# Kernel tuning notes

Measured on AMD Instinct MI355X. Metric: run time of the kernel, lower is better.

Reference implementation:

```python
import jax, jax.numpy as jnp
import numpy as np

V, D, H, L, E, DH, K, PMAX = 50257, 128, 4, 4, 8, 512, 2, 256
B, T = 8, 256


def setup_inputs() -> dict:
    key = jax.random.key(0)
    ks = jax.random.split(key, 10)
    s = 0.02
    def n(k, shape):
        return jax.random.normal(k, shape, jnp.float32) * s
    return dict(
        idx=jax.random.randint(ks[0], (B, T), 0, V),
        tok_emb=n(ks[1], (V, D)),
        pos_emb=n(ks[2], (PMAX, D)),
        ln1_g=jnp.ones((L, D), jnp.float32), ln1_b=jnp.zeros((L, D), jnp.float32),
        in_w=n(ks[3], (L, 3 * D, D)), in_b=jnp.zeros((L, 3 * D), jnp.float32),
        out_w=n(ks[4], (L, D, D)), out_b=jnp.zeros((L, D), jnp.float32),
        ln2_g=jnp.ones((L, D), jnp.float32), ln2_b=jnp.zeros((L, D), jnp.float32),
        gate_w=n(ks[5], (L, E, D)),
        w1=n(ks[6], (L, E, DH, D)),
        w2=n(ks[7], (L, E, D, DH)),
        lnf_g=jnp.ones((D,), jnp.float32), lnf_b=jnp.zeros((D,), jnp.float32),
        lm_w=n(ks[8], (V, D)),
    )


def _ln(x, g, b):
    mu = x.mean(-1, keepdims=True)
    var = jnp.var(x, -1, keepdims=True)
    return (x - mu) / jnp.sqrt(var + 1e-5) * g + b


def _moe(x, gw, w1, w2):
    # x: [N, D]; top-2 sparse MoE, computed densely per expert then combined.
    logits = x @ gw.T                              # [N, E]
    probs = jax.nn.softmax(logits, -1)
    topw, topi = jax.lax.top_k(probs, K)           # [N, K]
    topw = topw / topw.sum(-1, keepdims=True)
    we = (topw[..., None] * jax.nn.one_hot(topi, E, dtype=x.dtype)).sum(1)  # [N, E]
    h = jax.nn.silu(jnp.einsum('nd,ehd->neh', x, w1))   # [N, E, DH]
    y = jnp.einsum('neh,edh->ned', h, w2)               # [N, E, D]
    return jnp.einsum('ned,ne->nd', y, we)


def reference(idx, tok_emb, pos_emb, ln1_g, ln1_b, in_w, in_b, out_w, out_b,
              ln2_g, ln2_b, gate_w, w1, w2, lnf_g, lnf_b, lm_w):
    b, t = idx.shape
    x = tok_emb[idx] + pos_emb[:t]                 # [B, T, D]
    dh = D // H
    scale = 1.0 / np.sqrt(dh)
    for l in range(L):
        xl = _ln(x, ln1_g[l], ln1_b[l])
        qkv = xl @ in_w[l].T + in_b[l]
        q, k, v = jnp.split(qkv, 3, -1)
        q = q.reshape(b, t, H, dh)
        k = k.reshape(b, t, H, dh)
        v = v.reshape(b, t, H, dh)
        att = jax.nn.softmax(jnp.einsum('bqhd,bkhd->bhqk', q, k) * scale, -1)
        o = jnp.einsum('bhqk,bkhd->bqhd', att, v).reshape(b, t, D)
        x = x + o @ out_w[l].T + out_b[l]
        x2 = _ln(x, ln2_g[l], ln2_b[l]).reshape(b * t, D)
        x = x + _moe(x2, gate_w[l], w1[l], w2[l]).reshape(b, t, D)
    return _ln(x, lnf_g, lnf_b) @ lm_w.T           # [B, T, V]
```

## Files before the change

kernel.cpp:

```cpp
#include <hip/hip_runtime.h>
#include <math.h>

#define NTOK 2048
#define DD   128
#define NHEAD 4
#define DHEAD 32
#define NLAYER 4
#define NEXP 8
#define DHID 512
#define NVOCAB 50257
#define VPAD  50304
#define SEQ   256
#define NBATCH 8

typedef __attribute__((ext_vector_type(8))) short short8v;
typedef __attribute__((ext_vector_type(4))) float f32x4;

__device__ __forceinline__ unsigned short nm_bf16r(float f) {
  unsigned u = __float_as_uint(f);
  u += 0x7fffu + ((u >> 16) & 1u);
  return (unsigned short)(u >> 16);
}

__device__ __forceinline__ float nm_silu(float a) {
  return a / (1.f + __expf(-a));
}

template<int N4>
__device__ __forceinline__ float nm_dotv(const float* __restrict__ a,
                                         const float* __restrict__ w) {
  const float4* a4 = (const float4*)a;
  const float4* w4 = (const float4*)w;
  float sx = 0.f, sy = 0.f, sz = 0.f, sw = 0.f;
#pragma unroll 16
  for (int k = 0; k < N4; ++k) {
    float4 av = a4[k], wv = w4[k];
    sx = fmaf(av.x, wv.x, sx);
    sy = fmaf(av.y, wv.y, sy);
    sz = fmaf(av.z, wv.z, sz);
    sw = fmaf(av.w, wv.w, sw);
  }
  return (sx + sy) + (sz + sw);
}

#define C3_LMW 6438912ull
#define C3_W1  6963200ull
#define C3_ALL 7487488ull
#define CVTB   7312
__global__ __launch_bounds__(256) void nm_init(
    const int* __restrict__ idx, const float* __restrict__ tok,
    const float* __restrict__ pos, const float* __restrict__ g,
    const float* __restrict__ b, const float* __restrict__ lmw,
    const float* __restrict__ w1l3, const float* __restrict__ w2l3,
    float* __restrict__ x, float* __restrict__ xl,
    unsigned short* __restrict__ lmwb, unsigned short* __restrict__ w1b3,
    unsigned short* __restrict__ w2b3, int* __restrict__ zp) {
  int bid = blockIdx.x, tid = threadIdx.x;
  if (bid < CVTB) {
    size_t base = ((size_t)bid * 256 + tid) * 4;
    if (base < (size_t)NVOCAB * DD) {
      float4 v = *(const float4*)(lmw + base);
      ushort4 us = {nm_bf16r(v.x), nm_bf16r(v.y), nm_bf16r(v.z), nm_bf16r(v.w)};
      *(ushort4*)(lmwb + base) = us;
    } else if (base < C3_LMW) {
      ushort4 us = {0, 0, 0, 0};
      *(ushort4*)(lmwb + base) = us;
    } else if (base < C3_W1) {
      size_t j = base - C3_LMW;
      float4 v = *(const float4*)(w1l3 + j);
      ushort4 us = {nm_bf16r(v.x), nm_bf16r(v.y), nm_bf16r(v.z), nm_bf16r(v.w)};
      *(ushort4*)(w1b3 + j) = us;
    } else {
      size_t j = base - C3_W1;
      float4 v = *(const float4*)(w2l3 + j);
      ushort4 us = {nm_bf16r(v.x), nm_bf16r(v.y), nm_bf16r(v.z), nm_bf16r(v.w)};
      *(ushort4*)(w2b3 + j) = us;
    }
  } else if (bid < CVTB + NTOK / 4) {
    int n = (bid - CVTB) * 4 + (tid >> 6);
    int lane = tid & 63;
    int t = idx[n];
    float v0 = tok[(size_t)t * DD + lane]      + pos[(n % SEQ) * DD + lane];
    float v1 = tok[(size_t)t * DD + lane + 64] + pos[(n % SEQ) * DD + lane + 64];
    x[n * DD + lane]      = v0;
    x[n * DD + lane + 64] = v1;
    float s = v0 + v1;
#pragma unroll
    for (int o = 32; o > 0; o >>= 1) s += __shfl_xor(s, o, 64);
    float mu = s * (1.f / 128.f);
    float d0 = v0 - mu, d1 = v1 - mu;
    float q = d0 * d0 + d1 * d1;
#pragma unroll
    for (int o = 32; o > 0; o >>= 1) q += __shfl_xor(q, o, 64);
    float rstd = rsqrtf(q * (1.f / 128.f) + 1e-5f);
    xl[n * DD + lane]      = d0 * rstd * g[lane]      + b[lane];
    xl[n * DD + lane + 64] = d1 * rstd * g[lane + 64] + b[lane + 64];
  } else {
    if (tid < 72) zp[tid] = 0;
  }
}

__global__ void nm_embed_ln(const int* __restrict__ idx, const float* __restrict__ tok,
                            const float* __restrict__ pos, const float* __restrict__ g,
                            const float* __restrict__ b, float* __restrict__ x,
                            float* __restrict__ xlf) {
  int n = blockIdx.x, lane = threadIdx.x;
  int t = idx[n];
  float v0 = tok[(size_t)t * DD + lane]      + pos[(n % SEQ) * DD + lane];
  float v1 = tok[(size_t)t * DD + lane + 64] + pos[(n % SEQ) * DD + lane + 64];
  x[n * DD + lane]      = v0;
  x[n * DD + lane + 64] = v1;
  float s = v0 + v1;
#pragma unroll
  for (int o = 32; o > 0; o >>= 1) s += __shfl_xor(s, o, 64);
  float mu = s * (1.f / 128.f);
  float d0 = v0 - mu, d1 = v1 - mu;
  float q = d0 * d0 + d1 * d1;
#pragma unroll
  for (int o = 32; o > 0; o >>= 1) q += __shfl_xor(q, o, 64);
  float rstd = rsqrtf(q * (1.f / 128.f) + 1e-5f);
  xlf[n * DD + lane]      = d0 * rstd * g[lane]      + b[lane];
  xlf[n * DD + lane + 64] = d1 * rstd * g[lane + 64] + b[lane + 64];
}

__global__ void nm_ln(const float* __restrict__ in, const float* __restrict__ g,
                      const float* __restrict__ b, float* __restrict__ out) {
  int n = blockIdx.x, lane = threadIdx.x;
  float v0 = in[n * DD + lane], v1 = in[n * DD + lane + 64];
  float s = v0 + v1;
#pragma unroll
  for (int o = 32; o > 0; o >>= 1) s += __shfl_xor(s, o, 64);
  float mu = s * (1.f / 128.f);
  float d0 = v0 - mu, d1 = v1 - mu;
  float q = d0 * d0 + d1 * d1;
#pragma unroll
  for (int o = 32; o > 0; o >>= 1) q += __shfl_xor(q, o, 64);
  float rstd = rsqrtf(q * (1.f / 128.f) + 1e-5f);
  out[n * DD + lane]      = d0 * rstd * g[lane]      + b[lane];
  out[n * DD + lane + 64] = d1 * rstd * g[lane + 64] + b[lane + 64];
}

__global__ void nm_combine_ln(const float* __restrict__ yb, const int* __restrict__ posm,
                              const float* __restrict__ topw, float* __restrict__ x,
                              const float* __restrict__ g, const float* __restrict__ b,
                              float* __restrict__ xl, unsigned short* __restrict__ xb) {
  int n = blockIdx.x, lane = threadIdx.x;
  float w0 = topw[2 * n], w1 = topw[2 * n + 1];
  int p0 = posm[2 * n], p1 = posm[2 * n + 1];
  float v0 = x[n * DD + lane]      + w0 * yb[(size_t)p0 * DD + lane]
                                   + w1 * yb[(size_t)p1 * DD + lane];
  float v1 = x[n * DD + lane + 64] + w0 * yb[(size_t)p0 * DD + lane + 64]
                                   + w1 * yb[(size_t)p1 * DD + lane + 64];
  x[n * DD + lane]      = v0;
  x[n * DD + lane + 64] = v1;
  float s = v0 + v1;
#pragma unroll
  for (int o = 32; o > 0; o >>= 1) s += __shfl_xor(s, o, 64);
  float mu = s * (1.f / 128.f);
  float d0 = v0 - mu, d1 = v1 - mu;
  float q = d0 * d0 + d1 * d1;
#pragma unroll
  for (int o = 32; o > 0; o >>= 1) q += __shfl_xor(q, o, 64);
  float rstd = rsqrtf(q * (1.f / 128.f) + 1e-5f);
  float o0 = d0 * rstd * g[lane]      + b[lane];
  float o1 = d1 * rstd * g[lane + 64] + b[lane + 64];
  xl[n * DD + lane]      = o0;
  xl[n * DD + lane + 64] = o1;
  if (xb) {
    xb[n * DD + lane]      = nm_bf16r(o0);
    xb[n * DD + lane + 64] = nm_bf16r(o1);
  }
}

template<int F, int MT>
__global__ __launch_bounds__(256) void nm_gemm2(
    const float* __restrict__ A, const float* __restrict__ B,
    float* __restrict__ C, const float* __restrict__ bias,
    int M, int N, int K,
    const int* __restrict__ list, const int* __restrict__ cnt,
    const int* __restrict__ off) {
  constexpr bool GA = F & 1, SI = F & 2, BI = F & 4, GR = F & 16;
  constexpr int RG = MT / 64;
  __shared__ __align__(16) float As[64][MT + 4];
  __shared__ __align__(16) float Bs[64][68];
  int tid = threadIdx.x;
  int n0 = blockIdx.x * 64, m0 = blockIdx.y * MT;
  int Mloc = M, o = 0;
  const float* Bb = B;
  if constexpr (GR) {
    int e = blockIdx.z;
    Mloc = cnt[e];
    if (m0 >= Mloc) return;
    o = off[e];
    Bb = B + (size_t)e * (size_t)N * K;
  }
  int tm = tid & 15, tn = tid >> 4;
  float acc[RG * 4][4] = {};
  for (int kc = 0; kc < K; kc += 64) {
#pragma unroll
    for (int i = 0; i < RG * 4; ++i) {
      int f = tid + 256 * i;
      int r = f >> 4, c4 = f & 15;
      int mi = m0 + r;
      if (mi >= Mloc) mi = m0;
      const float* ar;
      if constexpr (GA) ar = A + (size_t)(list[o + mi] >> 1) * K;
      else              ar = A + (size_t)(o + mi) * K;
      float4 v = *(const float4*)(ar + kc + c4 * 4);
      int k = c4 * 4;
      As[k][r] = v.x; As[k + 1][r] = v.y; As[k + 2][r] = v.z; As[k + 3][r] = v.w;
    }
#pragma unroll
    for (int i = 0; i < 4; ++i) {
      int f = tid + 256 * i;
      int r = f >> 4, c4 = f & 15;
      const float* br = Bb + (size_t)(n0 + r) * K + kc + c4 * 4;
      float4 v = *(const float4*)br;
      int k = c4 * 4;
      Bs[k][r] = v.x; Bs[k + 1][r] = v.y; Bs[k + 2][r] = v.z; Bs[k + 3][r] = v.w;
    }
    __syncthreads();
#pragma unroll 16
    for (int k = 0; k < 64; ++k) {
      float4 b = *(const float4*)&Bs[k][tn * 4];
#pragma unroll
      for (int g2 = 0; g2 < RG; ++g2) {
        float4 a = *(const float4*)&As[k][g2 * 64 + tm * 4];
        acc[g2*4+0][0] = fmaf(a.x, b.x, acc[g2*4+0][0]);
        acc[g2*4+0][1] = fmaf(a.x, b.y, acc[g2*4+0][1]);
        acc[g2*4+0][2] = fmaf(a.x, b.z, acc[g2*4+0][2]);
        acc[g2*4+0][3] = fmaf(a.x, b.w, acc[g2*4+0][3]);
        acc[g2*4+1][0] = fmaf(a.y, b.x, acc[g2*4+1][0]);
        acc[g2*4+1][1] = fmaf(a.y, b.y, acc[g2*4+1][1]);
        acc[g2*4+1][2] = fmaf(a.y, b.z, acc[g2*4+1][2]);
        acc[g2*4+1][3] = fmaf(a.y, b.w, acc[g2*4+1][3]);
        acc[g2*4+2][0] = fmaf(a.z, b.x, acc[g2*4+2][0]);
        acc[g2*4+2][1] = fmaf(a.z, b.y, acc[g2*4+2][1]);
        acc[g2*4+2][2] = fmaf(a.z, b.z, acc[g2*4+2][2]);
        acc[g2*4+2][3] = fmaf(a.z, b.w, acc[g2*4+2][3]);
        acc[g2*4+3][0] = fmaf(a.w, b.x, acc[g2*4+3][0]);
        acc[g2*4+3][1] = fmaf(a.w, b.y, acc[g2*4+3][1]);
        acc[g2*4+3][2] = fmaf(a.w, b.z, acc[g2*4+3][2]);
        acc[g2*4+3][3] = fmaf(a.w, b.w, acc[g2*4+3][3]);
      }
    }
    __syncthreads();
  }
  float4 bv = {0.f, 0.f, 0.f, 0.f};
  if constexpr (BI) bv = *(const float4*)(bias + n0 + tn * 4);
#pragma unroll
  for (int g2 = 0; g2 < RG; ++g2) {
#pragma unroll
    for (int i = 0; i < 4; ++i) {
      int row = m0 + g2 * 64 + tm * 4 + i;
      if (GR && row >= Mloc) continue;
      float* cr = C + (size_t)(o + row) * N + n0 + tn * 4;
      float r0 = acc[g2 * 4 + i][0], r1 = acc[g2 * 4 + i][1];
      float r2 = acc[g2 * 4 + i][2], r3 = acc[g2 * 4 + i][3];
      if constexpr (BI) { r0 += bv.x; r1 += bv.y; r2 += bv.z; r3 += bv.w; }
      if constexpr (SI) { r0 = nm_silu(r0); r1 = nm_silu(r1); r2 = nm_silu(r2); r3 = nm_silu(r3); }
      float4 st = {r0, r1, r2, r3};
      *(float4*)cr = st;
    }
  }
}

template<int F, int KK>
__global__ __launch_bounds__(256) void nm_bgemm(
    const unsigned short* __restrict__ A, const unsigned short* __restrict__ B,
    float* __restrict__ Cf, unsigned short* __restrict__ Cb,
    const float* __restrict__ bias, int M, int N,
    const int* __restrict__ list, const int* __restrict__ cnt,
    const int* __restrict__ off) {
  constexpr bool GA = F & 1, SI = F & 2, BI = F & 4, SB = F & 8, GR = F & 16;
  int wave = threadIdx.x >> 6, lane = threadIdx.x & 63;
  int n0 = blockIdx.x * 32;
  int m0 = blockIdx.y * 128 + wave * 32;
  int Mloc = M, o = 0;
  const unsigned short* Bb = B;
  if constexpr (GR) {
    int e = blockIdx.z;
    Mloc = cnt[e];
    o = off[e];
    Bb = B + (size_t)e * (size_t)N * KK;
  }
  if (m0 >= Mloc) return;
  int lr = lane & 15, lk = (lane >> 4) * 8;
  const unsigned short* arow[2];
#pragma unroll
  for (int i = 0; i < 2; ++i) {
    int mi = m0 + i * 16 + lr;
    if (mi >= Mloc) mi = Mloc - 1;
    int r = GA ? (list[o + mi] >> 1) : (o + mi);
    arow[i] = A + (size_t)r * KK;
  }
  const unsigned short* brow[2] = { Bb + (size_t)(n0 + lr) * KK,
                                    Bb + (size_t)(n0 + 16 + lr) * KK };
  f32x4 acc[2][2] = {};
#pragma unroll
  for (int ks = 0; ks < KK / 32; ++ks) {
    int kb = ks * 32 + lk;
    short8v a0 = *(const short8v*)(arow[0] + kb);
    short8v a1 = *(const short8v*)(arow[1] + kb);
    short8v b0 = *(const short8v*)(brow[0] + kb);
    short8v b1 = *(const short8v*)(brow[1] + kb);
    acc[0][0] = __builtin_amdgcn_mfma_f32_16x16x32_bf16(a0, b0, acc[0][0], 0, 0, 0);
    acc[0][1] = __builtin_amdgcn_mfma_f32_16x16x32_bf16(a0, b1, acc[0][1], 0, 0, 0);
    acc[1][0] = __builtin_amdgcn_mfma_f32_16x16x32_bf16(a1, b0, acc[1][0], 0, 0, 0);
    acc[1][1] = __builtin_amdgcn_mfma_f32_16x16x32_bf16(a1, b1, acc[1][1], 0, 0, 0);
  }
  float bc[2] = {0.f, 0.f};
  if constexpr (BI) {
    bc[0] = bias[n0 + (lane & 15)];
    bc[1] = bias[n0 + 16 + (lane & 15)];
  }
#pragma unroll
  for (int i = 0; i < 2; ++i) {
    int rbase = m0 + i * 16 + (lane >> 4) * 4;
#pragma unroll
    for (int r = 0; r < 4; ++r) {
      int row = rbase + r;
      if (GR && row >= Mloc) continue;
#pragma unroll
      for (int j = 0; j < 2; ++j) {
        float v = acc[i][j][r];
        if constexpr (BI) v += bc[j];
        if constexpr (SI) v = nm_silu(v);
        int col = n0 + j * 16 + (lane & 15);
        if constexpr (SB) Cb[(size_t)(o + row) * N + col] = nm_bf16r(v);
        else              Cf[(size_t)(o + row) * N + col] = v;
      }
    }
  }
}

__global__ __launch_bounds__(256) void nm_oplng(
    const float* __restrict__ ao, const float* __restrict__ w,
    const float* __restrict__ bias, float* __restrict__ x,
    const float* __restrict__ g, const float* __restrict__ b,
    float* __restrict__ xl, unsigned short* __restrict__ xlb,
    const float* __restrict__ gw,
    int* __restrict__ topi, float* __restrict__ topw, int* __restrict__ cnt,
    int* __restrict__ ticket, int* __restrict__ off, int* __restrict__ list,
    int* __restrict__ posm) {
  __shared__ __align__(16) float As[64][36];
  __shared__ __align__(16) float Bs[64][132];
  __shared__ float Ls[32][9];
  __shared__ int doR;
  __shared__ int cv[NEXP], lcur[NEXP];
  int tid = threadIdx.x;
  int m0 = blockIdx.x * 32;
  int tm = tid >> 5, tn = tid & 31;
  float acc[4][4] = {};
  for (int kc = 0; kc < DD; kc += 64) {
#pragma unroll
    for (int i = 0; i < 2; ++i) {
      int ch = tid + 256 * i, r = ch >> 4, c4 = ch & 15;
      float4 v = *(const float4*)(ao + (size_t)(m0 + r) * DD + kc + c4 * 4);
      int k = c4 * 4;
      As[k][r] = v.x; As[k + 1][r] = v.y; As[k + 2][r] = v.z; As[k + 3][r] = v.w;
    }
#pragma unroll
    for (int i = 0; i < 8; ++i) {
      int ch = tid + 256 * i, r = ch >> 4, c4 = ch & 15;
      float4 v = *(const float4*)(w + (size_t)r * DD + kc + c4 * 4);
      int k = c4 * 4;
      Bs[k][r] = v.x; Bs[k + 1][r] = v.y; Bs[k + 2][r] = v.z; Bs[k + 3][r] = v.w;
    }
    __syncthreads();
#pragma unroll 8
    for (int k = 0; k < 64; ++k) {
      float4 a = *(const float4*)&As[k][tm * 4];
      float4 bb = *(const float4*)&Bs[k][tn * 4];
      acc[0][0] = fmaf(a.x, bb.x, acc[0][0]); acc[0][1] = fmaf(a.x, bb.y, acc[0][1]);
      acc[0][2] = fmaf(a.x, bb.z, acc[0][2]); acc[0][3] = fmaf(a.x, bb.w, acc[0][3]);
      acc[1][0] = fmaf(a.y, bb.x, acc[1][0]); acc[1][1] = fmaf(a.y, bb.y, acc[1][1]);
      acc[1][2] = fmaf(a.y, bb.z, acc[1][2]); acc[1][3] = fmaf(a.y, bb.w, acc[1][3]);
      acc[2][0] = fmaf(a.z, bb.x, acc[2][0]); acc[2][1] = fmaf(a.z, bb.y, acc[2][1]);
      acc[2][2] = fmaf(a.z, bb.z, acc[2][2]); acc[2][3] = fmaf(a.z, bb.w, acc[2][3]);
      acc[3][0] = fmaf(a.w, bb.x, acc[3][0]); acc[3][1] = fmaf(a.w, bb.y, acc[3][1]);
      acc[3][2] = fmaf(a.w, bb.z, acc[3][2]); acc[3][3] = fmaf(a.w, bb.w, acc[3][3]);
    }
    __syncthreads();
  }
  float4 bv = *(const float4*)(bias + tn * 4);
  float rr[4][4], s1[4], s2[4];
#pragma unroll
  for (int i = 0; i < 4; ++i) {
    int rw = m0 + tm * 4 + i;
    float4 xv = *(const float4*)(x + (size_t)rw * DD + tn * 4);
    float r0 = acc[i][0] + bv.x + xv.x;
    float r1 = acc[i][1] + bv.y + xv.y;
    float r2 = acc[i][2] + bv.z + xv.z;
    float r3 = acc[i][3] + bv.w + xv.w;
    rr[i][0] = r0; rr[i][1] = r1; rr[i][2] = r2; rr[i][3] = r3;
    float4 st = {r0, r1, r2, r3};
    *(float4*)(x + (size_t)rw * DD + tn * 4) = st;
    s1[i] = r0 + r1 + r2 + r3;
    s2[i] = r0 * r0 + r1 * r1 + r2 * r2 + r3 * r3;
  }
#pragma unroll
  for (int o = 16; o >= 1; o >>= 1) {
#pragma unroll
    for (int i = 0; i < 4; ++i) {
      s1[i] += __shfl_xor(s1[i], o, 64);
      s2[i] += __shfl_xor(s2[i], o, 64);
    }
  }
  float4 gv  = *(const float4*)(g + tn * 4);
  float4 bbv = *(const float4*)(b + tn * 4);
#pragma unroll
  for (int i = 0; i < 4; ++i) {
    int rw = m0 + tm * 4 + i;
    float mu = s1[i] * (1.f / 128.f);
    float var = s2[i] * (1.f / 128.f) - mu * mu;
    float rstd = rsqrtf(var + 1e-5f);
    float y0 = (rr[i][0] - mu) * rstd * gv.x + bbv.x;
    float y1 = (rr[i][1] - mu) * rstd * gv.y + bbv.y;
    float y2 = (rr[i][2] - mu) * rstd * gv.z + bbv.z;
    float y3 = (rr[i][3] - mu) * rstd * gv.w + bbv.w;
    float4 yv = {y0, y1, y2, y3};
    *(float4*)(xl + (size_t)rw * DD + tn * 4) = yv;
    if (xlb) {
      ushort4 us = {nm_bf16r(y0), nm_bf16r(y1), nm_bf16r(y2), nm_bf16r(y3)};
      *(ushort4*)(xlb + (size_t)rw * DD + tn * 4) = us;
    }
    *(float4*)&Bs[tm * 4 + i][tn * 4] = yv;
  }
  __syncthreads();
  int grow = tid >> 3, ge = tid & 7;
  const float4* xr = (const float4*)&Bs[grow][0];
  const float4* wr = (const float4*)(gw + (size_t)ge * DD);
  float sx = 0.f, sy = 0.f, sz = 0.f, sw = 0.f;
#pragma unroll
  for (int k2 = 0; k2 < 32; ++k2) {
    float4 a = xr[k2], w4 = wr[k2];
    sx = fmaf(a.x, w4.x, sx); sy = fmaf(a.y, w4.y, sy);
    sz = fmaf(a.z, w4.z, sz); sw = fmaf(a.w, w4.w, sw);
  }
  Ls[grow][ge] = (sx + sy) + (sz + sw);
  __syncthreads();
  if (ge == 0) {
    float gl[NEXP];
#pragma unroll
    for (int e = 0; e < NEXP; ++e) gl[e] = Ls[grow][e];
    int i0 = 0;
#pragma unroll
    for (int e = 1; e < NEXP; ++e) if (gl[e] > gl[i0]) i0 = e;
    int i1 = (i0 == 0) ? 1 : 0;
#pragma unroll
    for (int e = 0; e < NEXP; ++e) { if (e != i0 && gl[e] > gl[i1]) i1 = e; }
    float p1 = __expf(gl[i1] - gl[i0]);
    float inv = 1.f / (1.f + p1);
    int n = m0 + grow;
    topi[2 * n] = i0; topi[2 * n + 1] = i1;
    topw[2 * n] = inv; topw[2 * n + 1] = p1 * inv;
    atomicAdd(cnt + i0, 1);
    atomicAdd(cnt + i1, 1);
  }
  __syncthreads();
  if (tid == 0) {
    __threadfence();
    doR = (atomicAdd(ticket, 1) == 63);
    if (doR) __threadfence();
  }
  __syncthreads();
  if (doR) {
    if (tid < NEXP) cv[tid] = atomicAdd(cnt + tid, 0);
    __syncthreads();
    if (tid < NEXP) {
      int o2 = 0;
      for (int e = 0; e < tid; ++e) o2 += cv[e];
      lcur[tid] = o2;
      off[tid] = o2;
    }
    __syncthreads();
    for (int t = tid; t < 2 * NTOK; t += 256) {
      int e = topi[t];
      int p = atomicAdd(&lcur[e], 1);
      list[p] = t;
      posm[t] = p;
    }
  }
}

__global__ __launch_bounds__(256) void nm_attn3(const float* __restrict__ qkv,
                                                float* __restrict__ o) {
  __shared__ __align__(16) float smem[2 * SEQ * DHEAD];
  float4* K4 = (float4*)smem;
  float4* V4 = (float4*)(smem + SEQ * DHEAD);
  int bh = blockIdx.x;
  int b = bh >> 2, h = bh & 3;
  int qt = blockIdx.y;
  int tid = threadIdx.x;
  const float* base = qkv + (size_t)b * SEQ * 384;
  for (int f = tid; f < SEQ * 8; f += 256) {
    int t = f >> 3, c4 = f & 7;
    int pc = (c4 + (t >> 4)) & 7;
    K4[t * 8 + pc] = *(const float4*)(base + (size_t)t * 384 + 128 + h * DHEAD + c4 * 4);
    V4[t * 8 + pc] = *(const float4*)(base + (size_t)t * 384 + 256 + h * DHEAD + c4 * 4);
  }
  __syncthreads();
  int qi = tid >> 4, slot = tid & 15;
  int tq = qt * 16 + qi;
  float qv[DHEAD];
  const float4* q4 = (const float4*)(base + (size_t)tq * 384 + h * DHEAD);
#pragma unroll
  for (int k = 0; k < 8; ++k) {
    float4 v = q4[k];
    qv[4*k] = v.x; qv[4*k+1] = v.y; qv[4*k+2] = v.z; qv[4*k+3] = v.w;
  }
  float m = -1e30f, s = 0.f, acc[DHEAD];
#pragma unroll
  for (int d = 0; d < DHEAD; ++d) acc[d] = 0.f;
  const float scale = 0.17677669529663687f;
  int sw = slot & 7;
  for (int jj = 0; jj < 16; ++jj) {
    int j = slot * 16 + jj;
    float sc = 0.f;
#pragma unroll
    for (int k = 0; k < 8; ++k) {
      float4 v = K4[j * 8 + ((k + sw) & 7)];
      sc += qv[4*k]*v.x + qv[4*k+1]*v.y + qv[4*k+2]*v.z + qv[4*k+3]*v.w;
    }
    sc *= scale;
    float mn = fmaxf(m, sc);
    float f = __expf(m - mn), p = __expf(sc - mn);
    s = s * f + p;
#pragma unroll
    for (int k = 0; k < 8; ++k) {
      float4 v = V4[j * 8 + ((k + sw) & 7)];
      acc[4*k]   = acc[4*k]  * f + p * v.x;
      acc[4*k+1] = acc[4*k+1]* f + p * v.y;
      acc[4*k+2] = acc[4*k+2]* f + p * v.z;
      acc[4*k+3] = acc[4*k+3]* f + p * v.w;
    }
    m = mn;
  }
  __syncthreads();
  float* cb = smem;
  float* my = cb + (qi * 16 + slot) * 34;
#pragma unroll
  for (int d = 0; d < DHEAD; ++d) my[d] = acc[d];
  my[32] = m;
  my[33] = s;
  __syncthreads();
  int q2 = tid >> 4, dg = tid & 15;
  const float* qb = cb + q2 * 16 * 34;
  float M = qb[32];
#pragma unroll
  for (int t = 1; t < 16; ++t) M = fmaxf(M, qb[t * 34 + 32]);
  float S = 0.f, v0 = 0.f, v1 = 0.f;
#pragma unroll
  for (int t = 0; t < 16; ++t) {
    float w = __expf(qb[t * 34 + 32] - M);
    S += qb[t * 34 + 33] * w;
    v0 += w * qb[t * 34 + dg * 2];
    v1 += w * qb[t * 34 + dg * 2 + 1];
  }
  float inv = 1.f / S;
  float* orow = o + (size_t)(b * SEQ + qt * 16 + q2) * DD + h * DHEAD + dg * 2;
  orow[0] = v0 * inv;
  orow[1] = v1 * inv;
}

__global__ void nm_qkv(const float* __restrict__ xl, const float* __restrict__ w,
                       const float* __restrict__ bias, float* __restrict__ qkv) {
  __shared__ __align__(16) float xs[DD];
  int n = blockIdx.x, tid = threadIdx.x;
  xs[tid] = xl[n * DD + tid];
  __syncthreads();
#pragma unroll
  for (int jj = 0; jj < 3; ++jj) {
    int j = tid + jj * 128;
    qkv[(size_t)n * 384 + j] = nm_dotv<32>(xs, w + (size_t)j * DD) + bias[j];
  }
}

__global__ void nm_outproj(const float* __restrict__ ao, const float* __restrict__ w,
                           const float* __restrict__ bias, float* __restrict__ x) {
  __shared__ __align__(16) float os[DD];
  int n = blockIdx.x, tid = threadIdx.x;
  os[tid] = ao[n * DD + tid];
  __syncthreads();
  x[n * DD + tid] += nm_dotv<32>(os, w + (size_t)tid * DD) + bias[tid];
}

__global__ void nm_moe(const float* __restrict__ x2, const float* __restrict__ gw,
                       const float* __restrict__ w1, const float* __restrict__ w2,
                       float* __restrict__ x) {
  __shared__ __align__(16) float xs[DD];
  __shared__ __align__(16) float hs[DHID];
  __shared__ float gl[NEXP];
  __shared__ int   ei[2];
  __shared__ float ew[2];
  int n = blockIdx.x, tid = threadIdx.x;
  if (tid < DD) xs[tid] = x2[n * DD + tid];
  __syncthreads();
  if (tid < NEXP) gl[tid] = nm_dotv<32>(xs, gw + (size_t)tid * DD);
  __syncthreads();
  if (tid == 0) {
    int i0 = 0;
#pragma unroll
    for (int e = 1; e < NEXP; ++e) if (gl[e] > gl[i0]) i0 = e;
    int i1 = (i0 == 0) ? 1 : 0;
    for (int e = 0; e < NEXP; ++e) { if (e == i0) continue; if (gl[e] > gl[i1]) i1 = e; }
    float p1 = __expf(gl[i1] - gl[i0]);
    float inv = 1.f / (1.f + p1);
    ei[0] = i0; ei[1] = i1; ew[0] = inv; ew[1] = p1 * inv;
  }
  __syncthreads();
  float yacc = 0.f;
  for (int t2 = 0; t2 < 2; ++t2) {
    int e = ei[t2];
    float wt = ew[t2];
    const float* w1e = w1 + (size_t)e * DHID * DD;
#pragma unroll
    for (int jj = 0; jj < 2; ++jj) {
      int j = tid + jj * 256;
      float a = nm_dotv<32>(xs, w1e + (size_t)j * DD);
      hs[j] = nm_silu(a);
    }
    __syncthreads();
    if (tid < DD) yacc += wt * nm_dotv<128>(hs, w2 + ((size_t)e * DD + tid) * DHID);
    __syncthreads();
  }
  if (tid < DD) x[n * DD + tid] += yacc;
}

__device__ __forceinline__ short8v nm_cvt8(const float* p) {
  const float4* p4 = (const float4*)p;
  float4 a = p4[0], b = p4[1];
  short8v r;
  r[0] = (short)nm_bf16r(a.x); r[1] = (short)nm_bf16r(a.y);
  r[2] = (short)nm_bf16r(a.z); r[3] = (short)nm_bf16r(a.w);
  r[4] = (short)nm_bf16r(b.x); r[5] = (short)nm_bf16r(b.y);
  r[6] = (short)nm_bf16r(b.z); r[7] = (short)nm_bf16r(b.w);
  return r;
}

__global__ __launch_bounds__(256) void nm_lmhead_f32(
    const float* __restrict__ xf, const float* __restrict__ lmw,
    float* __restrict__ out) {
  int wave = threadIdx.x >> 6, lane = threadIdx.x & 63;
  int wr = wave >> 1, wc = wave & 1;
  int row0 = blockIdx.y * 128 + wr * 64;
  int col0 = blockIdx.x * 128 + wc * 64;
  int lr = lane & 15, lk = (lane >> 4) * 8;
  f32x4 acc[4][4] = {};
#pragma unroll
  for (int ks = 0; ks < 4; ++ks) {
    int kb = ks * 32 + lk;
    short8v a[4], b[4];
#pragma unroll
    for (int i = 0; i < 4; ++i)
      a[i] = nm_cvt8(xf + (size_t)(row0 + i * 16 + lr) * DD + kb);
#pragma unroll
    for (int j = 0; j < 4; ++j) {
      int c = col0 + j * 16 + lr;
      if (c < NVOCAB) b[j] = nm_cvt8(lmw + (size_t)c * DD + kb);
      else {
        short8v z;
#pragma unroll
        for (int e = 0; e < 8; ++e) z[e] = 0;
        b[j] = z;
      }
    }
#pragma unroll
    for (int i = 0; i < 4; ++i)
#pragma unroll
      for (int j = 0; j < 4; ++j)
        acc[i][j] = __builtin_amdgcn_mfma_f32_16x16x32_bf16(a[i], b[j], acc[i][j], 0, 0, 0);
  }
  int cr = (lane >> 4) * 4;
#pragma unroll
  for (int j = 0; j < 4; ++j) {
    int c = col0 + j * 16 + (lane & 15);
    if (c < NVOCAB) {
#pragma unroll
      for (int i = 0; i < 4; ++i)
#pragma unroll
        for (int r = 0; r < 4; ++r)
          out[(size_t)(row0 + i * 16 + cr + r) * NVOCAB + c] = acc[i][j][r];
    }
  }
}

__global__ __launch_bounds__(256) void nm_lmhead2(
    const unsigned short* __restrict__ xfb, const unsigned short* __restrict__ lmwb,
    float* __restrict__ out) {
  __shared__ __align__(16) unsigned char smem[132 * 128 * 4];
  unsigned short* Ab = (unsigned short*)smem;
  unsigned short* Bb = Ab + 128 * 128;
  int tid = threadIdx.x;
  int row0 = blockIdx.y * 128, col0 = blockIdx.x * 128;
#pragma unroll
  for (int i = 0; i < 8; ++i) {
    int ch = tid + i * 256;
    int r = ch >> 4, s = ch & 15;
    int sg = s ^ (r & 7);
    *(short8v*)&Ab[r * 128 + s * 8] =
        *(const short8v*)(xfb + (size_t)(row0 + r) * DD + sg * 8);
    *(short8v*)&Bb[r * 128 + s * 8] =
        *(const short8v*)(lmwb + (size_t)(col0 + r) * DD + sg * 8);
  }
  __syncthreads();
  int wave = tid >> 6, lane = tid & 63;
  int wr = wave >> 1, wc = wave & 1;
  int lr = lane & 15, hk = lane >> 4;
  f32x4 acc[4][4] = {};
#pragma unroll
  for (int ks = 0; ks < 4; ++ks) {
    int sg = ks * 4 + hk;
    int sx = (sg ^ (lr & 7)) * 8;
    short8v a[4], b[4];
#pragma unroll
    for (int i = 0; i < 4; ++i)
      a[i] = *(const short8v*)&Ab[(wr * 64 + i * 16 + lr) * 128 + sx];
#pragma unroll
    for (int j = 0; j < 4; ++j)
      b[j] = *(const short8v*)&Bb[(wc * 64 + j * 16 + lr) * 128 + sx];
#pragma unroll
    for (int i = 0; i < 4; ++i)
#pragma unroll
      for (int j = 0; j < 4; ++j)
        acc[i][j] = __builtin_amdgcn_mfma_f32_16x16x32_bf16(a[i], b[j], acc[i][j], 0, 0, 0);
  }
  __syncthreads();
  float* Cs = (float*)smem;
  int hi4 = hk * 4;
#pragma unroll
  for (int j = 0; j < 4; ++j)
#pragma unroll
    for (int i = 0; i < 4; ++i)
#pragma unroll
      for (int r = 0; r < 4; ++r)
        Cs[(wr * 64 + i * 16 + hi4 + r) * 132 + wc * 64 + j * 16 + lr] = acc[i][j][r];
  __syncthreads();
  bool full = (col0 + 128 <= NVOCAB);
#pragma unroll 4
  for (int rr = 0; rr < 32; ++rr) {
    int row = wave * 32 + rr;
    float v0 = Cs[row * 132 + lane];
    float v1 = Cs[row * 132 + 64 + lane];
    size_t base = (size_t)(row0 + row) * NVOCAB + col0;
    if (full) {
      out[base + lane] = v0;
      out[base + 64 + lane] = v1;
    } else {
      if (col0 + lane < NVOCAB)      out[base + lane] = v0;
      if (col0 + 64 + lane < NVOCAB) out[base + 64 + lane] = v1;
    }
  }
}

extern "C" void kernel_launch(void* const* d_in, const int* in_sizes, int n_in,
                              void* d_out, int out_size, void* d_ws, size_t ws_size,
                              hipStream_t stream) {
  const int*   idx   = (const int*)  d_in[0];
  const float* tok   = (const float*)d_in[1];
  const float* pos   = (const float*)d_in[2];
  const float* ln1g  = (const float*)d_in[3];
  const float* ln1b  = (const float*)d_in[4];
  const float* inw   = (const float*)d_in[5];
  const float* inb   = (const float*)d_in[6];
  const float* outw  = (const float*)d_in[7];
  const float* outb  = (const float*)d_in[8];
  const float* ln2g  = (const float*)d_in[9];
  const float* ln2b  = (const float*)d_in[10];
  const float* gatew = (const float*)d_in[11];
  const float* w1    = (const float*)d_in[12];
  const float* w2    = (const float*)d_in[13];
  const float* lnfg  = (const float*)d_in[14];
  const float* lnfb  = (const float*)d_in[15];
  const float* lmw   = (const float*)d_in[16];
  float* out = (float*)d_out;

  float* ws   = (float*)d_ws;
  float* x    = ws;
  float* xl   = x    + NTOK * DD;
  float* qkv  = xl   + NTOK * DD;
  float* ao   = qkv  + NTOK * 384;
  float* topw = ao   + NTOK * DD;
  float* H    = topw + 2 * NTOK;
  float* yb   = H    + 2 * NTOK * DHID;
  int*   topi = (int*)(yb + 2 * NTOK * DD);
  int*   list = topi + 2 * NTOK;
  int*   posm = list + 2 * NTOK;
  int*   cnt  = posm + 2 * NTOK;
  int*   offs = cnt  + NLAYER * NEXP;
  int*   tick = offs + NLAYER * NEXP;
  unsigned short* xlb  = (unsigned short*)(tick + 8);
  unsigned short* Hb   = xlb + NTOK * DD;
  unsigned short* xfb  = Hb  + 2 * NTOK * DHID;
  unsigned short* w1b3 = xfb + NTOK * DD;
  unsigned short* w2b3 = w1b3 + NEXP * DHID * DD;
  unsigned short* lmwb = w2b3 + NEXP * DD * DHID;
  const size_t need = (size_t)((char*)(lmwb + (size_t)VPAD * DD) - (char*)d_ws);
  const bool pre = (ws_size >= need);

  const float* w1l3 = w1 + (size_t)3 * NEXP * DHID * DD;
  const float* w2l3 = w2 + (size_t)3 * NEXP * DD * DHID;

  if (pre) {
    nm_init<<<CVTB + NTOK / 4 + 1, 256, 0, stream>>>(
        idx, tok, pos, ln1g, ln1b, lmw, w1l3, w2l3, x, xl, lmwb, w1b3, w2b3, cnt);
    for (int l = 0; l < NLAYER; ++l) {
      nm_gemm2<4, 64><<<dim3(384 / 64, NTOK / 64), 256, 0, stream>>>(
          xl, inw + (size_t)l * 384 * DD, qkv, inb + (size_t)l * 384,
          NTOK, 384, DD, nullptr, nullptr, nullptr);
      nm_attn3<<<dim3(NBATCH * NHEAD, SEQ / 16), 256, 0, stream>>>(qkv, ao);
      nm_oplng<<<NTOK / 32, 256, 0, stream>>>(
          ao, outw + (size_t)l * DD * DD, outb + (size_t)l * DD, x,
          ln2g + l * DD, ln2b + l * DD, xl, (l == 3) ? xlb : (unsigned short*)nullptr,
          gatew + (size_t)l * NEXP * DD, topi, topw, cnt + l * NEXP,
          tick + l, offs + l * NEXP, list, posm);
      int* cnt_l = cnt + l * NEXP;
      int* off_l = offs + l * NEXP;
      if (l < 3) {
        const float* w1l = w1 + (size_t)l * NEXP * DHID * DD;
        const float* w2l = w2 + (size_t)l * NEXP * DD * DHID;
        nm_gemm2<19, 64><<<dim3(DHID / 64, 2 * NTOK / 64, NEXP), 256, 0, stream>>>(
            xl, w1l, H, nullptr, 0, DHID, DD, list, cnt_l, off_l);
        nm_gemm2<16, 64><<<dim3(DD / 64, 2 * NTOK / 64, NEXP), 256, 0, stream>>>(
            H, w2l, yb, nullptr, 0, DD, DHID, nullptr, cnt_l, off_l);
      } else {
        nm_bgemm<27, 128><<<dim3(DHID / 32, 32, NEXP), 256, 0, stream>>>(
            xlb, w1b3, nullptr, Hb, nullptr, 0, DHID, list, cnt_l, off_l);
        nm_bgemm<16, 512><<<dim3(DD / 32, 32, NEXP), 256, 0, stream>>>(
            Hb, w2b3, yb, nullptr, nullptr, 0, DD, nullptr, cnt_l, off_l);
      }
      const float* gN = (l < NLAYER - 1) ? ln1g + (l + 1) * DD : lnfg;
      const float* bN = (l < NLAYER - 1) ? ln1b + (l + 1) * DD : lnfb;
      nm_combine_ln<<<NTOK, 64, 0, stream>>>(
          yb, posm, topw, x, gN, bN, xl,
          (l == NLAYER - 1) ? xfb : (unsigned short*)nullptr);
    }
    nm_lmhead2<<<dim3(VPAD / 128, NTOK / 128), 256, 0, stream>>>(xfb, lmwb, out);
  } else {
    nm_embed_ln<<<NTOK, 64, 0, stream>>>(idx, tok, pos, ln1g, ln1b, x, xl);
    for (int l = 0; l < NLAYER; ++l) {
      nm_qkv<<<NTOK, 128, 0, stream>>>(xl, inw + (size_t)l * 384 * DD,
                                       inb + (size_t)l * 384, qkv);
      nm_attn3<<<dim3(NBATCH * NHEAD, SEQ / 16), 256, 0, stream>>>(qkv, ao);
      nm_outproj<<<NTOK, 128, 0, stream>>>(ao, outw + (size_t)l * DD * DD,
                                           outb + (size_t)l * DD, x);
      nm_ln<<<NTOK, 64, 0, stream>>>(x, ln2g + l * DD, ln2b + l * DD, xl);
      nm_moe<<<NTOK, 256, 0, stream>>>(xl, gatew + (size_t)l * NEXP * DD,
                                       w1 + (size_t)l * NEXP * DHID * DD,
                                       w2 + (size_t)l * NEXP * DD * DHID, x);
      const float* gN = (l < NLAYER - 1) ? ln1g + (l + 1) * DD : lnfg;
      const float* bN = (l < NLAYER - 1) ? ln1b + (l + 1) * DD : lnfb;
      nm_ln<<<NTOK, 64, 0, stream>>>(x, gN, bN, xl);
    }
    nm_lmhead_f32<<<dim3(VPAD / 128, NTOK / 128), 256, 0, stream>>>(xl, lmw, out);
  }
}
```

Baseline: 766.9 us.

## Fuse MoE combine and next-layer LayerNorm into the QKV projection kernel

Replaces the separate combine+LN kernel and the following QKV GEMM with one templated kernel. It applies the top-2 expert combine, computes LayerNorm over 32-token tiles in registers, and computes the 384-wide QKV projection from shared memory. Mode 0 handles the first layer from the precomputed LN output, and mode 2 handles the final LN with bf16 output. This removes one launch per layer and the global round trip of the normalized activations. In exchange the projection uses a scalar fp32 dot product per output instead of the tiled GEMM, and LayerNorm now uses a one-pass variance formula.

```diff
diff --git a/kernel.cpp b/kernel.cpp
--- a/kernel.cpp
+++ b/kernel.cpp
@@ -100,75 +100,100 @@
   }
 }
 
-__global__ void nm_embed_ln(const int* __restrict__ idx, const float* __restrict__ tok,
-                            const float* __restrict__ pos, const float* __restrict__ g,
-                            const float* __restrict__ b, float* __restrict__ x,
-                            float* __restrict__ xlf) {
-  int n = blockIdx.x, lane = threadIdx.x;
-  int t = idx[n];
-  float v0 = tok[(size_t)t * DD + lane]      + pos[(n % SEQ) * DD + lane];
-  float v1 = tok[(size_t)t * DD + lane + 64] + pos[(n % SEQ) * DD + lane + 64];
-  x[n * DD + lane]      = v0;
-  x[n * DD + lane + 64] = v1;
-  float s = v0 + v1;
-#pragma unroll
-  for (int o = 32; o > 0; o >>= 1) s += __shfl_xor(s, o, 64);
-  float mu = s * (1.f / 128.f);
-  float d0 = v0 - mu, d1 = v1 - mu;
-  float q = d0 * d0 + d1 * d1;
-#pragma unroll
-  for (int o = 32; o > 0; o >>= 1) q += __shfl_xor(q, o, 64);
-  float rstd = rsqrtf(q * (1.f / 128.f) + 1e-5f);
-  xlf[n * DD + lane]      = d0 * rstd * g[lane]      + b[lane];
-  xlf[n * DD + lane + 64] = d1 * rstd * g[lane + 64] + b[lane + 64];
-}
-
-__global__ void nm_ln(const float* __restrict__ in, const float* __restrict__ g,
-                      const float* __restrict__ b, float* __restrict__ out) {
-  int n = blockIdx.x, lane = threadIdx.x;
-  float v0 = in[n * DD + lane], v1 = in[n * DD + lane + 64];
-  float s = v0 + v1;
-#pragma unroll
-  for (int o = 32; o > 0; o >>= 1) s += __shfl_xor(s, o, 64);
-  float mu = s * (1.f / 128.f);
-  float d0 = v0 - mu, d1 = v1 - mu;
-  float q = d0 * d0 + d1 * d1;
-#pragma unroll
-  for (int o = 32; o > 0; o >>= 1) q += __shfl_xor(q, o, 64);
-  float rstd = rsqrtf(q * (1.f / 128.f) + 1e-5f);
-  out[n * DD + lane]      = d0 * rstd * g[lane]      + b[lane];
-  out[n * DD + lane + 64] = d1 * rstd * g[lane + 64] + b[lane + 64];
-}
-
-__global__ void nm_combine_ln(const float* __restrict__ yb, const int* __restrict__ posm,
-                              const float* __restrict__ topw, float* __restrict__ x,
-                              const float* __restrict__ g, const float* __restrict__ b,
-                              float* __restrict__ xl, unsigned short* __restrict__ xb) {
-  int n = blockIdx.x, lane = threadIdx.x;
-  float w0 = topw[2 * n], w1 = topw[2 * n + 1];
-  int p0 = posm[2 * n], p1 = posm[2 * n + 1];
-  float v0 = x[n * DD + lane]      + w0 * yb[(size_t)p0 * DD + lane]
-                                   + w1 * yb[(size_t)p1 * DD + lane];
-  float v1 = x[n * DD + lane + 64] + w0 * yb[(size_t)p0 * DD + lane + 64]
-                                   + w1 * yb[(size_t)p1 * DD + lane + 64];
-  x[n * DD + lane]      = v0;
-  x[n * DD + lane + 64] = v1;
-  float s = v0 + v1;
-#pragma unroll
-  for (int o = 32; o > 0; o >>= 1) s += __shfl_xor(s, o, 64);
-  float mu = s * (1.f / 128.f);
-  float d0 = v0 - mu, d1 = v1 - mu;
-  float q = d0 * d0 + d1 * d1;
-#pragma unroll
-  for (int o = 32; o > 0; o >>= 1) q += __shfl_xor(q, o, 64);
-  float rstd = rsqrtf(q * (1.f / 128.f) + 1e-5f);
-  float o0 = d0 * rstd * g[lane]      + b[lane];
-  float o1 = d1 * rstd * g[lane + 64] + b[lane + 64];
-  xl[n * DD + lane]      = o0;
-  xl[n * DD + lane + 64] = o1;
-  if (xb) {
-    xb[n * DD + lane]      = nm_bf16r(o0);
-    xb[n * DD + lane + 64] = nm_bf16r(o1);
+template<int MODE>
+__global__ __launch_bounds__(256) void nm_cqkv(
+    const float* __restrict__ yb, const int* __restrict__ posm,
+    const float* __restrict__ topw, float* __restrict__ x,
+    const float* __restrict__ xlin, const float* __restrict__ g,
+    const float* __restrict__ b, unsigned short* __restrict__ xfb,
+    const float* __restrict__ w, const float* __restrict__ bias,
+    float* __restrict__ qkv) {
+  __shared__ __align__(16) float xs[32][132];
+  __shared__ __align__(16) float qs[(MODE < 2) ? 32 * 388 : 4];
+  int tid = threadIdx.x;
+  int n0 = blockIdx.x * 32;
+  int r = tid >> 3, p = tid & 7;
+  int n = n0 + r;
+  float4 a0, a1, a2, a3;
+  if constexpr (MODE == 0) {
+    const float* xr = xlin + (size_t)n * DD + p * 16;
+    a0 = *(const float4*)(xr + 0);  a1 = *(const float4*)(xr + 4);
+    a2 = *(const float4*)(xr + 8);  a3 = *(const float4*)(xr + 12);
+#pragma unroll
+    for (int i = 0; i < 4; ++i) {
+      ((float4*)&xs[r][p * 16])[i] = (i == 0) ? a0 : (i == 1) ? a1 : (i == 2) ? a2 : a3;
+    }
+  } else {
+    float* xr = x + (size_t)n * DD + p * 16;
+    a0 = *(const float4*)(xr + 0);  a1 = *(const float4*)(xr + 4);
+    a2 = *(const float4*)(xr + 8);  a3 = *(const float4*)(xr + 12);
+    float w0 = topw[2 * n], w1 = topw[2 * n + 1];
+    int p0 = posm[2 * n], p1 = posm[2 * n + 1];
+    const float* y0 = yb + (size_t)p0 * DD + p * 16;
+    const float* y1 = yb + (size_t)p1 * DD + p * 16;
+#pragma unroll
+    for (int i = 0; i < 4; ++i) {
+      float4 u0 = ((const float4*)y0)[i];
+      float4 u1 = ((const float4*)y1)[i];
+      float4* ai = (i == 0) ? &a0 : (i == 1) ? &a1 : (i == 2) ? &a2 : &a3;
+      ai->x += w0 * u0.x + w1 * u1.x;
+      ai->y += w0 * u0.y + w1 * u1.y;
+      ai->z += w0 * u0.z + w1 * u1.z;
+      ai->w += w0 * u0.w + w1 * u1.w;
+    }
+    if constexpr (MODE == 1) {
+      ((float4*)xr)[0] = a0; ((float4*)xr)[1] = a1;
+      ((float4*)xr)[2] = a2; ((float4*)xr)[3] = a3;
+    }
+    float s1 = (a0.x + a0.y + a0.z + a0.w) + (a1.x + a1.y + a1.z + a1.w)
+             + (a2.x + a2.y + a2.z + a2.w) + (a3.x + a3.y + a3.z + a3.w);
+    float s2 = a0.x*a0.x + a0.y*a0.y + a0.z*a0.z + a0.w*a0.w
+             + a1.x*a1.x + a1.y*a1.y + a1.z*a1.z + a1.w*a1.w
+             + a2.x*a2.x + a2.y*a2.y + a2.z*a2.z + a2.w*a2.w
+             + a3.x*a3.x + a3.y*a3.y + a3.z*a3.z + a3.w*a3.w;
+#pragma unroll
+    for (int o = 4; o >= 1; o >>= 1) {
+      s1 += __shfl_xor(s1, o, 8);
+      s2 += __shfl_xor(s2, o, 8);
+    }
+    float mu = s1 * (1.f / 128.f);
+    float var = s2 * (1.f / 128.f) - mu * mu;
+    float rstd = rsqrtf(var + 1e-5f);
+    const float4* gp = (const float4*)(g + p * 16);
+    const float4* bp = (const float4*)(b + p * 16);
+#pragma unroll
+    for (int i = 0; i < 4; ++i) {
+      float4 gv = gp[i], bv = bp[i];
+      float4* ai = (i == 0) ? &a0 : (i == 1) ? &a1 : (i == 2) ? &a2 : &a3;
+      float4 yv = {(ai->x - mu) * rstd * gv.x + bv.x,
+                   (ai->y - mu) * rstd * gv.y + bv.y,
+                   (ai->z - mu) * rstd * gv.z + bv.z,
+                   (ai->w - mu) * rstd * gv.w + bv.w};
+      if constexpr (MODE == 2) {
+        ushort4 us = {nm_bf16r(yv.x), nm_bf16r(yv.y), nm_bf16r(yv.z), nm_bf16r(yv.w)};
+        *(ushort4*)(xfb + (size_t)n * DD + p * 16 + i * 4) = us;
+      } else {
+        ((float4*)&xs[r][p * 16])[i] = yv;
+      }
+    }
+  }
+  if constexpr (MODE == 2) return;
+  __syncthreads();
+  float* qsf = (float*)qs;
+#pragma unroll 8
+  for (int i = 0; i < 48; ++i) {
+    int pp = i * 256 + tid;
+    int col = pp >> 5, tk = pp & 31;
+    float v = nm_dotv<32>(&xs[tk][0], w + (size_t)col * DD) + bias[col];
+    qsf[tk * 388 + col] = v;
+  }
+  __syncthreads();
+#pragma unroll
+  for (int i = 0; i < 12; ++i) {
+    int e4 = i * 256 + tid;
+    int tk = e4 / 96, c4 = e4 % 96;
+    float4 v = *(const float4*)&qsf[tk * 388 + c4 * 4];
+    *(float4*)(qkv + (size_t)(n0 + tk) * 384 + c4 * 4) = v;
   }
 }
 
@@ -562,6 +587,46 @@
   float* orow = o + (size_t)(b * SEQ + qt * 16 + q2) * DD + h * DHEAD + dg * 2;
   orow[0] = v0 * inv;
   orow[1] = v1 * inv;
+}
+
+__global__ void nm_embed_ln(const int* __restrict__ idx, const float* __restrict__ tok,
+                            const float* __restrict__ pos, const float* __restrict__ g,
+                            const float* __restrict__ b, float* __restrict__ x,
+                            float* __restrict__ xlf) {
+  int n = blockIdx.x, lane = threadIdx.x;
+  int t = idx[n];
+  float v0 = tok[(size_t)t * DD + lane]      + pos[(n % SEQ) * DD + lane];
+  float v1 = tok[(size_t)t * DD + lane + 64] + pos[(n % SEQ) * DD + lane + 64];
+  x[n * DD + lane]      = v0;
+  x[n * DD + lane + 64] = v1;
+  float s = v0 + v1;
+#pragma unroll
+  for (int o = 32; o > 0; o >>= 1) s += __shfl_xor(s, o, 64);
+  float mu = s * (1.f / 128.f);
+  float d0 = v0 - mu, d1 = v1 - mu;
+  float q = d0 * d0 + d1 * d1;
+#pragma unroll
+  for (int o = 32; o > 0; o >>= 1) q += __shfl_xor(q, o, 64);
+  float rstd = rsqrtf(q * (1.f / 128.f) + 1e-5f);
+  xlf[n * DD + lane]      = d0 * rstd * g[lane]      + b[lane];
+  xlf[n * DD + lane + 64] = d1 * rstd * g[lane + 64] + b[lane + 64];
+}
+
+__global__ void nm_ln(const float* __restrict__ in, const float* __restrict__ g,
+                      const float* __restrict__ b, float* __restrict__ out) {
+  int n = blockIdx.x, lane = threadIdx.x;
+  float v0 = in[n * DD + lane], v1 = in[n * DD + lane + 64];
+  float s = v0 + v1;
+#pragma unroll
+  for (int o = 32; o > 0; o >>= 1) s += __shfl_xor(s, o, 64);
+  float mu = s * (1.f / 128.f);
+  float d0 = v0 - mu, d1 = v1 - mu;
+  float q = d0 * d0 + d1 * d1;
+#pragma unroll
+  for (int o = 32; o > 0; o >>= 1) q += __shfl_xor(q, o, 64);
+  float rstd = rsqrtf(q * (1.f / 128.f) + 1e-5f);
+  out[n * DD + lane]      = d0 * rstd * g[lane]      + b[lane];
+  out[n * DD + lane + 64] = d1 * rstd * g[lane + 64] + b[lane + 64];
 }
 
 __global__ void nm_qkv(const float* __restrict__ xl, const float* __restrict__ w,
@@ -805,10 +870,10 @@
   if (pre) {
     nm_init<<<CVTB + NTOK / 4 + 1, 256, 0, stream>>>(
         idx, tok, pos, ln1g, ln1b, lmw, w1l3, w2l3, x, xl, lmwb, w1b3, w2b3, cnt);
+    nm_cqkv<0><<<NTOK / 32, 256, 0, stream>>>(
+        nullptr, nullptr, nullptr, x, xl, nullptr, nullptr, nullptr,
+        inw, inb, qkv);
     for (int l = 0; l < NLAYER; ++l) {
-      nm_gemm2<4, 64><<<dim3(384 / 64, NTOK / 64), 256, 0, stream>>>(
-          xl, inw + (size_t)l * 384 * DD, qkv, inb + (size_t)l * 384,
-          NTOK, 384, DD, nullptr, nullptr, nullptr);
       nm_attn3<<<dim3(NBATCH * NHEAD, SEQ / 16), 256, 0, stream>>>(qkv, ao);
       nm_oplng<<<NTOK / 32, 256, 0, stream>>>(
           ao, outw + (size_t)l * DD * DD, outb + (size_t)l * DD, x,
@@ -830,11 +895,15 @@
         nm_bgemm<16, 512><<<dim3(DD / 32, 32, NEXP), 256, 0, stream>>>(
             Hb, w2b3, yb, nullptr, nullptr, 0, DD, nullptr, cnt_l, off_l);
       }
-      const float* gN = (l < NLAYER - 1) ? ln1g + (l + 1) * DD : lnfg;
-      const float* bN = (l < NLAYER - 1) ? ln1b + (l + 1) * DD : lnfb;
-      nm_combine_ln<<<NTOK, 64, 0, stream>>>(
-          yb, posm, topw, x, gN, bN, xl,
-          (l == NLAYER - 1) ? xfb : (unsigned short*)nullptr);
+      if (l < NLAYER - 1) {
+        nm_cqkv<1><<<NTOK / 32, 256, 0, stream>>>(
+            yb, posm, topw, x, nullptr, ln1g + (l + 1) * DD, ln1b + (l + 1) * DD,
+            nullptr, inw + (size_t)(l + 1) * 384 * DD, inb + (size_t)(l + 1) * 384,
+            qkv);
+      } else {
+        nm_cqkv<2><<<NTOK / 32, 256, 0, stream>>>(
+            yb, posm, topw, x, nullptr, lnfg, lnfb, xfb, nullptr, nullptr, nullptr);
+      }
     }
     nm_lmhead2<<<dim3(VPAD / 128, NTOK / 128), 256, 0, stream>>>(xfb, lmwb, out);
   } else {
```

After: 996.7 us. 1.3x slower.
